# Kernel optimization log

Hardware: AMD Instinct MI355X
Metric: run time of the kernel (lower is better)

The kernel has to match this reference:

```python
import jax, jax.numpy as jnp
import numpy as np

B, S, D, H, DH = 8, 1024, 768, 12, 64
INIT_STD = 0.02
IGNORE = -100000.0


def setup_inputs() -> dict:
    key = jax.random.key(0)
    ks = jax.random.split(key, 5)
    return {
        "normalized_resid_pre": jax.random.normal(ks[0], (B, S, D), dtype=jnp.float32),
        "W_Q": jax.random.normal(ks[1], (H, D, DH), dtype=jnp.float32) * INIT_STD,
        "b_Q": jnp.zeros((H, DH), dtype=jnp.float32),
        "W_K": jax.random.normal(ks[2], (H, D, DH), dtype=jnp.float32) * INIT_STD,
        "b_K": jnp.zeros((H, DH), dtype=jnp.float32),
        "W_V": jax.random.normal(ks[3], (H, D, DH), dtype=jnp.float32) * INIT_STD,
        "b_V": jnp.zeros((H, DH), dtype=jnp.float32),
        "W_O": jax.random.normal(ks[4], (H, DH, D), dtype=jnp.float32) * INIT_STD,
        "b_O": jnp.zeros((D,), dtype=jnp.float32),
    }


def reference(normalized_resid_pre, W_Q, b_Q, W_K, b_K, W_V, b_V, W_O, b_O):
    x = normalized_resid_pre  # [B,S,D]
    q = jnp.einsum('bsd,hde->bshe', x, W_Q) + b_Q  # [B,S,H,DH]
    k = jnp.einsum('bsd,hde->bshe', x, W_K) + b_K
    v = jnp.einsum('bsd,hde->bshe', x, W_V) + b_V
    scores = jnp.einsum('bqhe,bkhe->bhqk', q, k) / jnp.sqrt(jnp.float32(DH))
    causal = jnp.triu(jnp.ones((S, S), dtype=bool), k=1)  # True above diagonal
    scores = jnp.where(causal, jnp.float32(IGNORE), scores)
    pattern = jax.nn.softmax(scores, axis=-1)  # [B,H,S,S]
    z = jnp.einsum('bhqk,bkhe->bqhe', pattern, v)  # [B,S,H,DH]
    attn_out = jnp.einsum('bqhe,hed->bqd', z, W_O) + b_O  # [B,S,D]
    return attn_out
```

## Files before the change

### kernel.cpp

```cpp
#include <hip/hip_runtime.h>
#include <hip/hip_bf16.h>
#include <stdint.h>

#define BB 8
#define SS 1024
#define DD 768
#define HH 12
#define DHH 64
#define BS (BB*SS)
#define NQKV (3*HH*DHH)

typedef __attribute__((ext_vector_type(8))) short bf16x8;
typedef __attribute__((ext_vector_type(4))) float f32x4;
typedef __attribute__((ext_vector_type(4))) unsigned int u32x4;

typedef const __attribute__((address_space(1))) unsigned int gu32;
typedef __attribute__((address_space(3))) unsigned int lu32;

static __device__ __forceinline__ unsigned short f2bf(float f) {
    union { float f; unsigned int u; } v; v.f = f;
    unsigned int u = v.u;
    unsigned int r = (u + 0x7fffu + ((u >> 16) & 1u)) >> 16;
    return (unsigned short)r;
}

static __device__ __forceinline__ unsigned int cvt_pk_bf16(float lo, float hi) {
    unsigned int r;
    asm("v_cvt_pk_bf16_f32 %0, %1, %2" : "=v"(r) : "v"(lo), "v"(hi));
    return r;
}


__global__ void k_f32_to_bf16(const float* __restrict__ in, unsigned short* __restrict__ out, int n) {
    int i = (blockIdx.x * 256 + threadIdx.x) * 4;
    if (i + 3 < n) {
        float4 v = *reinterpret_cast<const float4*>(in + i);
        ushort4 o;
        o.x = f2bf(v.x); o.y = f2bf(v.y); o.z = f2bf(v.z); o.w = f2bf(v.w);
        *reinterpret_cast<ushort4*>(out + i) = o;
    } else {
        for (; i < n; ++i) out[i] = f2bf(in[i]);
    }
}

__global__ void k_transpose_wqkv(const float* __restrict__ wq, const float* __restrict__ wk,
                                 const float* __restrict__ wv, unsigned short* __restrict__ wt) {
    __shared__ float tl[64][65];
    int rt = blockIdx.x;
    int z = blockIdx.y;
    int mat = z / 12, h = z - mat * 12;
    const float* src = ((mat == 0) ? wq : (mat == 1) ? wk : wv) + (size_t)h * 768 * 64;
    int d0 = rt * 64;
    int t = threadIdx.x;
    int row = t >> 4, c4 = (t & 15) * 4;
    #pragma unroll
    for (int p = 0; p < 4; ++p) {
        int d = p * 16 + row;
        float4 v = *reinterpret_cast<const float4*>(&src[(size_t)(d0 + d) * 64 + c4]);
        tl[d][c4 + 0] = v.x; tl[d][c4 + 1] = v.y; tl[d][c4 + 2] = v.z; tl[d][c4 + 3] = v.w;
    }
    __syncthreads();
    unsigned short* dstb = wt + ((size_t)(mat * 768 + h * 64)) * 768;
    #pragma unroll
    for (int p = 0; p < 4; ++p) {
        int e = p * 16 + row;
        ushort4 o;
        o.x = f2bf(tl[c4 + 0][e]); o.y = f2bf(tl[c4 + 1][e]);
        o.z = f2bf(tl[c4 + 2][e]); o.w = f2bf(tl[c4 + 3][e]);
        *reinterpret_cast<ushort4*>(&dstb[(size_t)e * 768 + d0 + c4]) = o;
    }
}

__global__ void k_transpose_wo(const float* __restrict__ wo, unsigned short* __restrict__ wot) {
    __shared__ float tl[64][65];
    int r0 = blockIdx.x * 64;
    int c0 = blockIdx.y * 64;
    int t = threadIdx.x;
    int row = t >> 4, c4 = (t & 15) * 4;
    #pragma unroll
    for (int p = 0; p < 4; ++p) {
        int r = p * 16 + row;
        float4 v = *reinterpret_cast<const float4*>(&wo[(size_t)(r0 + r) * 768 + c0 + c4]);
        tl[r][c4 + 0] = v.x; tl[r][c4 + 1] = v.y; tl[r][c4 + 2] = v.z; tl[r][c4 + 3] = v.w;
    }
    __syncthreads();
    #pragma unroll
    for (int p = 0; p < 4; ++p) {
        int c = p * 16 + row;
        ushort4 o;
        o.x = f2bf(tl[c4 + 0][c]); o.y = f2bf(tl[c4 + 1][c]);
        o.z = f2bf(tl[c4 + 2][c]); o.w = f2bf(tl[c4 + 3][c]);
        *reinterpret_cast<ushort4*>(&wot[(size_t)(c0 + c) * 768 + r0 + c4]) = o;
    }
}

__global__ void k_transpose_v(const unsigned short* __restrict__ vb, unsigned short* __restrict__ vtb) {
    __shared__ unsigned short tl[64][68];
    int s0 = blockIdx.x * 64;
    int bh = blockIdx.y;
    const unsigned short* src = vb + (size_t)bh * SS * DHH;
    unsigned short* dst = vtb + (size_t)bh * DHH * SS;
    int t = threadIdx.x;
    #pragma unroll
    for (int i = 0; i < 16; ++i) {
        int idx = t + i * 256;
        int sl = idx >> 6, e = idx & 63;
        tl[sl][e] = src[(size_t)(s0 + sl) * DHH + e];
    }
    __syncthreads();
    #pragma unroll
    for (int i = 0; i < 16; ++i) {
        int idx = t + i * 256;
        int e = idx >> 6, sl = idx & 63;
        dst[(size_t)e * SS + s0 + sl] = tl[sl][e];
    }
}


__launch_bounds__(256)
__global__ void k_gemm_qkv(const unsigned short* __restrict__ xb,
                           const unsigned short* __restrict__ wt,
                           const float* __restrict__ bq, const float* __restrict__ bk,
                           const float* __restrict__ bv,
                           unsigned short* __restrict__ qb,
                           unsigned short* __restrict__ kb,
                           unsigned short* __restrict__ vb) {
    __shared__ unsigned short As[128 * 32];
    __shared__ unsigned short Bs[128 * 32];
    int r0 = blockIdx.x * 128;
    int c0 = blockIdx.y * 128;
    int t = threadIdx.x;
    int w = t >> 6, l = t & 63;
    int lr = l & 15, lg = l >> 4;
    int wr = w >> 1, wc = w & 1;
    int srow = l >> 2, sko = (l & 3) * 8;

    f32x4 acc[4][4] = {};
    for (int k0 = 0; k0 < DD; k0 += 32) {
        __syncthreads();
        #pragma unroll
        for (int c = 0; c < 2; ++c) {
            int seg = w * 2 + c;
            int row = seg * 16 + srow;
            __builtin_amdgcn_global_load_lds(
                (gu32*)(xb + (size_t)(r0 + row) * DD + k0 + sko),
                (lu32*)&As[seg * 512], 16, 0, 0);
            __builtin_amdgcn_global_load_lds(
                (gu32*)(wt + (size_t)(c0 + row) * DD + k0 + sko),
                (lu32*)&Bs[seg * 512], 16, 0, 0);
        }
        __syncthreads();
        bf16x8 af[4], bfr[4];
        #pragma unroll
        for (int m = 0; m < 4; ++m)
            af[m] = *reinterpret_cast<const bf16x8*>(&As[(wr * 64 + m * 16 + lr) * 32 + lg * 8]);
        #pragma unroll
        for (int n = 0; n < 4; ++n)
            bfr[n] = *reinterpret_cast<const bf16x8*>(&Bs[(wc * 64 + n * 16 + lr) * 32 + lg * 8]);
        #pragma unroll
        for (int m = 0; m < 4; ++m)
            #pragma unroll
            for (int n = 0; n < 4; ++n)
                acc[m][n] = __builtin_amdgcn_mfma_f32_16x16x32_bf16(af[m], bfr[n], acc[m][n], 0, 0, 0);
    }
    #pragma unroll
    for (int n = 0; n < 4; ++n) {
        int c = c0 + wc * 64 + n * 16 + lr;
        int mat = c / 768;
        int within = c - mat * 768;
        int h = within >> 6, e = within & 63;
        const float* bptr = (mat == 0) ? bq : (mat == 1) ? bk : bv;
        float bias = bptr[within];
        unsigned short* dst = (mat == 0) ? qb : (mat == 1) ? kb : vb;
        #pragma unroll
        for (int m = 0; m < 4; ++m) {
            #pragma unroll
            for (int i = 0; i < 4; ++i) {
                int r = r0 + wr * 64 + m * 16 + lg * 4 + i;
                int b_ = r >> 10, s_ = r & 1023;
                dst[(((size_t)(b_ * HH + h)) * SS + s_) * DHH + e] = f2bf(acc[m][n][i] + bias);
            }
        }
    }
}


#define PW 34

__launch_bounds__(256, 3)
__global__ void k_attn(const unsigned short* __restrict__ qb,
                       const unsigned short* __restrict__ kb,
                       const unsigned short* __restrict__ vtb,
                       unsigned short* __restrict__ zb) {
    __shared__ unsigned short Ks[2][64 * 64];
    __shared__ unsigned short Vs[2][64 * 64];
    __shared__ unsigned int Pl[4][16 * PW];
    int id = blockIdx.x;
    int xcd = id & 7;
    int j = id >> 3;
    int bh = xcd * 12 + (j % 12);
    int qi = 15 - (j / 12);
    int q0 = qi * 64;

    int t = threadIdx.x, w = t >> 6, l = t & 63;
    int lr = l & 15, lg = l >> 4;
    const unsigned short* Qh = qb + (size_t)bh * SS * DHH;
    const unsigned short* Kh = kb + (size_t)bh * SS * DHH;
    const unsigned short* Vt = vtb + (size_t)bh * DHH * SS;
    int b_ = bh / HH, h = bh - b_ * HH;
    unsigned int* Pw = &Pl[w][0];

    int sr8 = l >> 3;
    int sc = ((l & 7) ^ sr8) * 8;

    auto STAGE = [&](int buf, int kbase) {
        #pragma unroll
        for (int c = 0; c < 2; ++c) {
            int seg = w * 2 + c;
            int row = seg * 8 + sr8;
            __builtin_amdgcn_global_load_lds(
                (gu32*)(Kh + (size_t)(kbase + row) * DHH + sc),
                (lu32*)&Ks[buf][seg * 512], 16, 0, 0);
            __builtin_amdgcn_global_load_lds(
                (gu32*)(Vt + (size_t)row * SS + kbase + sc),
                (lu32*)&Vs[buf][seg * 512], 16, 0, 0);
        }
    };

    int qabs = q0 + w * 16 + lr;
    STAGE(0, 0);
    bf16x8 qf[2];
    qf[0] = *reinterpret_cast<const bf16x8*>(Qh + (size_t)qabs * DHH + lg * 8);
    qf[1] = *reinterpret_cast<const bf16x8*>(Qh + (size_t)qabs * DHH + 32 + lg * 8);

    float m_r = -3.0e38f, l_r = 0.f;
    f32x4 zacc[4] = {};
    __syncthreads();

    for (int kt = 0; kt <= qi; ++kt) {
        int k0 = kt * 64;
        int cur = kt & 1;
        if (kt < qi) STAGE(cur ^ 1, k0 + 64);

        f32x4 sac[4] = {};
        __builtin_amdgcn_s_setprio(1);
        #pragma unroll
        for (int ks = 0; ks < 2; ++ks) {
            #pragma unroll
            for (int ct = 0; ct < 4; ++ct) {
                bf16x8 kfr = *reinterpret_cast<const bf16x8*>(
                    &Ks[cur][(ct * 16 + lr) * 64 + (((ks * 4 + lg) ^ (lr & 7)) * 8)]);
                sac[ct] = __builtin_amdgcn_mfma_f32_16x16x32_bf16(kfr, qf[ks], sac[ct], 0, 0, 0);
            }
        }
        __builtin_amdgcn_s_setprio(0);
        bool diag = (kt == qi);
        float sv[4][4];
        float pm = -3.0e38f;
        #pragma unroll
        for (int ct = 0; ct < 4; ++ct) {
            #pragma unroll
            for (int i = 0; i < 4; ++i) {
                float x = sac[ct][i] * 0.125f;
                if (diag) {
                    int kabs = k0 + ct * 16 + lg * 4 + i;
                    if (kabs > qabs) x = -3.0e38f;
                }
                sv[ct][i] = x;
                pm = fmaxf(pm, x);
            }
        }
        pm = fmaxf(pm, __shfl_xor(pm, 16));
        pm = fmaxf(pm, __shfl_xor(pm, 32));

        if (!__all(pm <= m_r + 8.f)) {
            float mn = fmaxf(m_r, pm);
            float alpha = __expf(m_r - mn);
            m_r = mn;
            l_r *= alpha;
            float aC[4];
            #pragma unroll
            for (int i = 0; i < 4; ++i) aC[i] = __shfl(alpha, lg * 4 + i);
            #pragma unroll
            for (int et = 0; et < 4; ++et)
                #pragma unroll
                for (int i = 0; i < 4; ++i) zacc[et][i] *= aC[i];
        }

        float ps = 0.f;
        #pragma unroll
        for (int ct = 0; ct < 4; ++ct) {
            float p0 = __expf(sv[ct][0] - m_r);
            float p1 = __expf(sv[ct][1] - m_r);
            float p2 = __expf(sv[ct][2] - m_r);
            float p3 = __expf(sv[ct][3] - m_r);
            ps += (p0 + p1) + (p2 + p3);
            unsigned int pk0 = cvt_pk_bf16(p0, p1);
            unsigned int pk1 = cvt_pk_bf16(p2, p3);
            *reinterpret_cast<uint2*>(&Pw[lr * PW + ct * 8 + lg * 2]) = make_uint2(pk0, pk1);
        }
        ps += __shfl_xor(ps, 16);
        ps += __shfl_xor(ps, 32);
        l_r += ps;

        __builtin_amdgcn_s_setprio(1);
        #pragma unroll
        for (int ks = 0; ks < 2; ++ks) {
            bf16x8 pa = *reinterpret_cast<const bf16x8*>(&Pw[lr * PW + ks * 16 + lg * 4]);
            #pragma unroll
            for (int et = 0; et < 4; ++et) {
                bf16x8 vf = *reinterpret_cast<const bf16x8*>(
                    &Vs[cur][(et * 16 + lr) * 64 + (((ks * 4 + lg) ^ (lr & 7)) * 8)]);
                zacc[et] = __builtin_amdgcn_mfma_f32_16x16x32_bf16(pa, vf, zacc[et], 0, 0, 0);
            }
        }
        __builtin_amdgcn_s_setprio(0);
        __syncthreads();
    }

    float lC[4];
    #pragma unroll
    for (int i = 0; i < 4; ++i) lC[i] = __shfl(l_r, lg * 4 + i);
    #pragma unroll
    for (int et = 0; et < 4; ++et) {
        #pragma unroll
        for (int i = 0; i < 4; ++i) {
            int r = q0 + w * 16 + lg * 4 + i;
            float z = zacc[et][i] / lC[i];
            zb[((size_t)(b_ * SS + r)) * DD + h * DHH + et * 16 + lr] = f2bf(z);
        }
    }
}


__launch_bounds__(256)
__global__ void k_gemm_out(const unsigned short* __restrict__ zb,
                           const unsigned short* __restrict__ wot,
                           const float* __restrict__ bo,
                           float* __restrict__ out) {
    __shared__ unsigned short As[128 * 32];
    __shared__ unsigned short Bs[128 * 32];
    int r0 = blockIdx.x * 128;
    int c0 = blockIdx.y * 128;
    int t = threadIdx.x;
    int w = t >> 6, l = t & 63;
    int lr = l & 15, lg = l >> 4;
    int wr = w >> 1, wc = w & 1;
    int srow = l >> 2, sko = (l & 3) * 8;

    f32x4 acc[4][4] = {};
    for (int k0 = 0; k0 < DD; k0 += 32) {
        __syncthreads();
        #pragma unroll
        for (int c = 0; c < 2; ++c) {
            int seg = w * 2 + c;
            int row = seg * 16 + srow;
            __builtin_amdgcn_global_load_lds(
                (gu32*)(zb + (size_t)(r0 + row) * DD + k0 + sko),
                (lu32*)&As[seg * 512], 16, 0, 0);
            __builtin_amdgcn_global_load_lds(
                (gu32*)(wot + (size_t)(c0 + row) * DD + k0 + sko),
                (lu32*)&Bs[seg * 512], 16, 0, 0);
        }
        __syncthreads();
        bf16x8 af[4], bfr[4];
        #pragma unroll
        for (int m = 0; m < 4; ++m)
            af[m] = *reinterpret_cast<const bf16x8*>(&As[(wr * 64 + m * 16 + lr) * 32 + lg * 8]);
        #pragma unroll
        for (int n = 0; n < 4; ++n)
            bfr[n] = *reinterpret_cast<const bf16x8*>(&Bs[(wc * 64 + n * 16 + lr) * 32 + lg * 8]);
        #pragma unroll
        for (int m = 0; m < 4; ++m)
            #pragma unroll
            for (int n = 0; n < 4; ++n)
                acc[m][n] = __builtin_amdgcn_mfma_f32_16x16x32_bf16(af[m], bfr[n], acc[m][n], 0, 0, 0);
    }
    #pragma unroll
    for (int n = 0; n < 4; ++n) {
        int c = c0 + wc * 64 + n * 16 + lr;
        float bias = bo[c];
        #pragma unroll
        for (int m = 0; m < 4; ++m) {
            #pragma unroll
            for (int i = 0; i < 4; ++i) {
                int r = r0 + wr * 64 + m * 16 + lg * 4 + i;
                out[(size_t)r * DD + c] = acc[m][n][i] + bias;
            }
        }
    }
}


extern "C" void kernel_launch(void* const* d_in, const int* in_sizes, int n_in,
                              void* d_out, int out_size, void* d_ws, size_t ws_size,
                              hipStream_t stream) {
    const float* x  = (const float*)d_in[0];
    const float* wq = (const float*)d_in[1];
    const float* bq = (const float*)d_in[2];
    const float* wk = (const float*)d_in[3];
    const float* bk = (const float*)d_in[4];
    const float* wv = (const float*)d_in[5];
    const float* bv = (const float*)d_in[6];
    const float* wo = (const float*)d_in[7];
    const float* bo = (const float*)d_in[8];
    float* out = (float*)d_out;

    char* ws = (char*)d_ws;
    size_t off = 0;
    auto alloc = [&](size_t bytes) -> char* {
        char* p = ws + off;
        off += (bytes + 255) & ~(size_t)255;
        return p;
    };
    unsigned short* xb   = (unsigned short*)alloc((size_t)BS * DD * 2);
    unsigned short* wt   = (unsigned short*)alloc((size_t)NQKV * DD * 2);
    unsigned short* wot  = (unsigned short*)alloc((size_t)DD * DD * 2);
    unsigned short* qb   = (unsigned short*)alloc((size_t)BB * HH * SS * DHH * 2);
    unsigned short* kb   = (unsigned short*)alloc((size_t)BB * HH * SS * DHH * 2);
    unsigned short* vb   = (unsigned short*)alloc((size_t)BB * HH * SS * DHH * 2);
    unsigned short* vtb  = (unsigned short*)alloc((size_t)BB * HH * SS * DHH * 2);
    unsigned short* zb   = (unsigned short*)alloc((size_t)BS * DD * 2);
    (void)ws_size; (void)in_sizes; (void)n_in; (void)out_size;

    k_f32_to_bf16<<<dim3((BS * DD) / (256 * 4)), dim3(256), 0, stream>>>(x, xb, BS * DD);
    k_transpose_wqkv<<<dim3(12, 36), dim3(256), 0, stream>>>(wq, wk, wv, wt);
    k_transpose_wo<<<dim3(12, 12), dim3(256), 0, stream>>>(wo, wot);
    k_gemm_qkv<<<dim3(BS / 128, NQKV / 128), dim3(256), 0, stream>>>(xb, wt, bq, bk, bv, qb, kb, vb);
    k_transpose_v<<<dim3(SS / 64, BB * HH), dim3(256), 0, stream>>>(vb, vtb);
    k_attn<<<dim3(16 * 96), dim3(256), 0, stream>>>(qb, kb, vtb, zb);
    k_gemm_out<<<dim3(BS / 128, DD / 128), dim3(256), 0, stream>>>(zb, wot, bo, out);
}
```

Before: 124.1 us.

## Fuse V transpose into QKV GEMM epilogue and use 128-row query tiles in attention

The QKV GEMM epilogue now writes V straight into the transposed [bh][e][s] layout with 4-element vector stores. This removes the separate V transpose kernel and its intermediate buffer. The attention kernel moves to 512-thread blocks covering 128 query rows with 8 waves, so each K/V tile staged into LDS is shared by twice as many waves. This halves the block count and per-block staging work, but it coarsens the causal load imbalance and raises LDS and register use per block.

```diff
diff --git a/kernel.cpp b/kernel.cpp
--- a/kernel.cpp
+++ b/kernel.cpp
@@ -94,28 +94,6 @@
     }
 }
 
-__global__ void k_transpose_v(const unsigned short* __restrict__ vb, unsigned short* __restrict__ vtb) {
-    __shared__ unsigned short tl[64][68];
-    int s0 = blockIdx.x * 64;
-    int bh = blockIdx.y;
-    const unsigned short* src = vb + (size_t)bh * SS * DHH;
-    unsigned short* dst = vtb + (size_t)bh * DHH * SS;
-    int t = threadIdx.x;
-    #pragma unroll
-    for (int i = 0; i < 16; ++i) {
-        int idx = t + i * 256;
-        int sl = idx >> 6, e = idx & 63;
-        tl[sl][e] = src[(size_t)(s0 + sl) * DHH + e];
-    }
-    __syncthreads();
-    #pragma unroll
-    for (int i = 0; i < 16; ++i) {
-        int idx = t + i * 256;
-        int e = idx >> 6, sl = idx & 63;
-        dst[(size_t)e * SS + s0 + sl] = tl[sl][e];
-    }
-}
-
 
 __launch_bounds__(256)
 __global__ void k_gemm_qkv(const unsigned short* __restrict__ xb,
@@ -124,7 +102,7 @@
                            const float* __restrict__ bv,
                            unsigned short* __restrict__ qb,
                            unsigned short* __restrict__ kb,
-                           unsigned short* __restrict__ vb) {
+                           unsigned short* __restrict__ vtb) {
     __shared__ unsigned short As[128 * 32];
     __shared__ unsigned short Bs[128 * 32];
     int r0 = blockIdx.x * 128;
@@ -171,14 +149,22 @@
         int h = within >> 6, e = within & 63;
         const float* bptr = (mat == 0) ? bq : (mat == 1) ? bk : bv;
         float bias = bptr[within];
-        unsigned short* dst = (mat == 0) ? qb : (mat == 1) ? kb : vb;
         #pragma unroll
         for (int m = 0; m < 4; ++m) {
-            #pragma unroll
-            for (int i = 0; i < 4; ++i) {
-                int r = r0 + wr * 64 + m * 16 + lg * 4 + i;
-                int b_ = r >> 10, s_ = r & 1023;
-                dst[(((size_t)(b_ * HH + h)) * SS + s_) * DHH + e] = f2bf(acc[m][n][i] + bias);
+            int r = r0 + wr * 64 + m * 16 + lg * 4;
+            int b_ = r >> 10, s_ = r & 1023;
+            if (mat == 2) {
+                ushort4 o;
+                o.x = f2bf(acc[m][n][0] + bias);
+                o.y = f2bf(acc[m][n][1] + bias);
+                o.z = f2bf(acc[m][n][2] + bias);
+                o.w = f2bf(acc[m][n][3] + bias);
+                *reinterpret_cast<ushort4*>(&vtb[((size_t)(b_ * HH + h) * DHH + e) * SS + s_]) = o;
+            } else {
+                unsigned short* dst = (mat == 0) ? qb : kb;
+                #pragma unroll
+                for (int i = 0; i < 4; ++i)
+                    dst[(((size_t)(b_ * HH + h)) * SS + s_ + i) * DHH + e] = f2bf(acc[m][n][i] + bias);
             }
         }
     }
@@ -187,20 +173,21 @@
 
 #define PW 34
 
-__launch_bounds__(256, 3)
+__launch_bounds__(512, 6)
 __global__ void k_attn(const unsigned short* __restrict__ qb,
                        const unsigned short* __restrict__ kb,
                        const unsigned short* __restrict__ vtb,
                        unsigned short* __restrict__ zb) {
     __shared__ unsigned short Ks[2][64 * 64];
     __shared__ unsigned short Vs[2][64 * 64];
-    __shared__ unsigned int Pl[4][16 * PW];
+    __shared__ unsigned int Pl[8][16 * PW];
     int id = blockIdx.x;
     int xcd = id & 7;
     int j = id >> 3;
     int bh = xcd * 12 + (j % 12);
-    int qi = 15 - (j / 12);
-    int q0 = qi * 64;
+    int qi = 7 - (j / 12);
+    int q0 = qi * 128;
+    int nkt = 2 * qi + 2;
 
     int t = threadIdx.x, w = t >> 6, l = t & 63;
     int lr = l & 15, lg = l >> 4;
@@ -212,19 +199,15 @@
 
     int sr8 = l >> 3;
     int sc = ((l & 7) ^ sr8) * 8;
+    int srow = w * 8 + sr8;
 
     auto STAGE = [&](int buf, int kbase) {
-        #pragma unroll
-        for (int c = 0; c < 2; ++c) {
-            int seg = w * 2 + c;
-            int row = seg * 8 + sr8;
-            __builtin_amdgcn_global_load_lds(
-                (gu32*)(Kh + (size_t)(kbase + row) * DHH + sc),
-                (lu32*)&Ks[buf][seg * 512], 16, 0, 0);
-            __builtin_amdgcn_global_load_lds(
-                (gu32*)(Vt + (size_t)row * SS + kbase + sc),
-                (lu32*)&Vs[buf][seg * 512], 16, 0, 0);
-        }
+        __builtin_amdgcn_global_load_lds(
+            (gu32*)(Kh + (size_t)(kbase + srow) * DHH + sc),
+            (lu32*)&Ks[buf][w * 512], 16, 0, 0);
+        __builtin_amdgcn_global_load_lds(
+            (gu32*)(Vt + (size_t)srow * SS + kbase + sc),
+            (lu32*)&Vs[buf][w * 512], 16, 0, 0);
     };
 
     int qabs = q0 + w * 16 + lr;
@@ -237,10 +220,10 @@
     f32x4 zacc[4] = {};
     __syncthreads();
 
-    for (int kt = 0; kt <= qi; ++kt) {
+    for (int kt = 0; kt < nkt; ++kt) {
         int k0 = kt * 64;
         int cur = kt & 1;
-        if (kt < qi) STAGE(cur ^ 1, k0 + 64);
+        if (kt + 1 < nkt) STAGE(cur ^ 1, k0 + 64);
 
         f32x4 sac[4] = {};
         __builtin_amdgcn_s_setprio(1);
@@ -254,7 +237,7 @@
             }
         }
         __builtin_amdgcn_s_setprio(0);
-        bool diag = (kt == qi);
+        bool maybeMask = (kt >= 2 * qi);
         float sv[4][4];
         float pm = -3.0e38f;
         #pragma unroll
@@ -262,7 +245,7 @@
             #pragma unroll
             for (int i = 0; i < 4; ++i) {
                 float x = sac[ct][i] * 0.125f;
-                if (diag) {
+                if (maybeMask) {
                     int kabs = k0 + ct * 16 + lg * 4 + i;
                     if (kabs > qabs) x = -3.0e38f;
                 }
@@ -418,7 +401,6 @@
     unsigned short* wot  = (unsigned short*)alloc((size_t)DD * DD * 2);
     unsigned short* qb   = (unsigned short*)alloc((size_t)BB * HH * SS * DHH * 2);
     unsigned short* kb   = (unsigned short*)alloc((size_t)BB * HH * SS * DHH * 2);
-    unsigned short* vb   = (unsigned short*)alloc((size_t)BB * HH * SS * DHH * 2);
     unsigned short* vtb  = (unsigned short*)alloc((size_t)BB * HH * SS * DHH * 2);
     unsigned short* zb   = (unsigned short*)alloc((size_t)BS * DD * 2);
     (void)ws_size; (void)in_sizes; (void)n_in; (void)out_size;
@@ -426,8 +408,7 @@
     k_f32_to_bf16<<<dim3((BS * DD) / (256 * 4)), dim3(256), 0, stream>>>(x, xb, BS * DD);
     k_transpose_wqkv<<<dim3(12, 36), dim3(256), 0, stream>>>(wq, wk, wv, wt);
     k_transpose_wo<<<dim3(12, 12), dim3(256), 0, stream>>>(wo, wot);
-    k_gemm_qkv<<<dim3(BS / 128, NQKV / 128), dim3(256), 0, stream>>>(xb, wt, bq, bk, bv, qb, kb, vb);
-    k_transpose_v<<<dim3(SS / 64, BB * HH), dim3(256), 0, stream>>>(vb, vtb);
-    k_attn<<<dim3(16 * 96), dim3(256), 0, stream>>>(qb, kb, vtb, zb);
+    k_gemm_qkv<<<dim3(BS / 128, NQKV / 128), dim3(256), 0, stream>>>(xb, wt, bq, bk, bv, qb, kb, vtb);
+    k_attn<<<dim3(768), dim3(512), 0, stream>>>(qb, kb, vtb, zb);
     k_gemm_out<<<dim3(BS / 128, DD / 128), dim3(256), 0, stream>>>(zb, wot, bo, out);
 }
```

Result: slower. 134.0 us (+7.9%).
